# Optimization experiments

Measured on AMD Instinct MI355X. Metric: run time of the kernel, lower is better.

## Reference

```python
import jax, jax.numpy as jnp
import numpy as np

NUM_CLASSES = 21
IGNORE_INDEX = 30
ALPHA = 0.25
GAMMA = 2.0
EPS = 1e-8        # numerical-stability eps added to softmax in lasd_f
ONEHOT_EPS = 1e-6  # eps added inside label_to_one_hot_label (its default)


def _lasd(logits, target):
    # logits: (N, C, H, W), target: (N, H, W) int in [0, C-1]
    p = jax.nn.softmax(logits, axis=1) + EPS                # (N,C,H,W)
    # torch.std(dim=1) uses the unbiased estimator (ddof=1)
    sigma = jnp.std(p, axis=1, ddof=1)                       # (N,H,W)
    # min_max_scale_f: global MinMaxScaler over all elements (detached in torch)
    smin = jnp.min(sigma)
    smax = jnp.max(sigma)
    sigma = (sigma - smin) / (smax - smin)
    sigma = jax.lax.stop_gradient(sigma)  # torch path goes through .detach().numpy()
    beta = 1.0 / jnp.exp(sigma) + 1.0                        # (N,H,W)
    # one-hot with ignore_index+1 channels (+eps), then keep first NUM_CLASSES
    one_hot = jax.nn.one_hot(target, IGNORE_INDEX + 1, axis=1,
                             dtype=logits.dtype) + ONEHOT_EPS  # (N,31,H,W)
    one_hot = one_hot[:, :NUM_CLASSES]                        # (N,C,H,W)
    focal = -ALPHA * (1.0 - p) ** GAMMA * jnp.log(p)          # (N,C,H,W)
    focal = focal * beta[:, None, :, :]
    loss_tmp = one_hot * focal
    # reduction='mean': mean over batch then mean over rest == overall mean
    loss = jnp.mean(loss_tmp)
    return loss, sigma


def setup_inputs() -> dict:
    key = jax.random.key(0)
    k1, k2 = jax.random.split(key)
    inp = jax.random.normal(k1, (8, NUM_CLASSES, 512, 512), dtype=jnp.float32)
    tgt = jax.random.randint(k2, (8, 512, 512), 0, NUM_CLASSES, dtype=jnp.int32)
    return {"input": inp, "target": tgt}


def reference(input, target):
    return _lasd(input, target)
```

## Files before the change

### kernel.cpp

```cpp
#include <hip/hip_runtime.h>

#define NCLS 21
#define HW (512 * 512)
#define HW2 (HW / 2)
#define NB 8
#define NPIX (NB * HW)
#define NPIX2 (NPIX / 2)
#define NPIX4 (NPIX / 4)
#define NBLK1 (NPIX2 / 256)
#define NBLK2 (NPIX4 / 256)
#define TOTAL_ELEMS ((long long)NPIX * NCLS)


__global__ __launch_bounds__(256) void lasd_pass1(const float2* __restrict__ in2,
                                                  const int2* __restrict__ tgt2,
                                                  float2* __restrict__ sigraw2,
                                                  float2* __restrict__ S2,
                                                  float* __restrict__ bmin,
                                                  float* __restrict__ bmax) {
    int j = blockIdx.x * 256 + threadIdx.x;
    int b = j >> 17;
    int p2 = j & (HW2 - 1);
    const float2* base = in2 + ((size_t)(b * NCLS) << 17) + p2;

    float2 x[NCLS];
#pragma unroll
    for (int c = 0; c < NCLS; ++c) x[c] = base[(size_t)c << 17];

    float s0 = 0.f, s1 = 0.f;
#pragma unroll
    for (int c = 0; c < NCLS; ++c) { s0 += __expf(x[c].x); s1 += __expf(x[c].y); }
    float inv0 = 1.0f / s0, inv1 = 1.0f / s1;
    float ls0 = __logf(s0), ls1 = __logf(s1);

    int2 tt = tgt2[j];

    float sp0 = 0, sp1 = 0, q0 = 0, q1 = 0, F0 = 0, F1 = 0, ft0 = 0, ft1 = 0;
#pragma unroll
    for (int c = 0; c < NCLS; ++c) {
        float p0 = __expf(x[c].x) * inv0 + 1e-8f;
        float p1 = __expf(x[c].y) * inv1 + 1e-8f;
        float om0 = 1.0f - p0, om1 = 1.0f - p1;
        float f0 = -0.25f * om0 * om0 * (x[c].x - ls0);
        float f1 = -0.25f * om1 * om1 * (x[c].y - ls1);
        sp0 += p0; sp1 += p1;
        q0 = fmaf(p0, p0, q0); q1 = fmaf(p1, p1, q1);
        F0 += f0; F1 += f1;
        if (c == tt.x) ft0 = f0;
        if (c == tt.y) ft1 = f1;
    }

    float var0 = fmaxf(q0 - sp0 * sp0 * (1.0f / 21.0f), 0.0f);
    float var1 = fmaxf(q1 - sp1 * sp1 * (1.0f / 21.0f), 0.0f);
    float sig0 = sqrtf(var0 * (1.0f / 20.0f));
    float sig1 = sqrtf(var1 * (1.0f / 20.0f));

    float2 sg; sg.x = sig0; sg.y = sig1;
    sigraw2[j] = sg;
    float2 Sv; Sv.x = ft0 + 1e-6f * F0; Sv.y = ft1 + 1e-6f * F1;
    S2[j] = Sv;

    float lmin = fminf(sig0, sig1), lmax = fmaxf(sig0, sig1);
#pragma unroll
    for (int off = 32; off > 0; off >>= 1) {
        lmin = fminf(lmin, __shfl_down(lmin, off));
        lmax = fmaxf(lmax, __shfl_down(lmax, off));
    }
    __shared__ float smn[4], smx[4];
    int wid = threadIdx.x >> 6, lane = threadIdx.x & 63;
    if (lane == 0) { smn[wid] = lmin; smx[wid] = lmax; }
    __syncthreads();
    if (threadIdx.x == 0) {
        bmin[blockIdx.x] = fminf(fminf(smn[0], smn[1]), fminf(smn[2], smn[3]));
        bmax[blockIdx.x] = fmaxf(fmaxf(smx[0], smx[1]), fmaxf(smx[2], smx[3]));
    }
}

__global__ __launch_bounds__(256) void lasd_reduce_mm(const float* __restrict__ bmin,
                                                      const float* __restrict__ bmax,
                                                      float2* __restrict__ mm) {
    float a = 1e30f, z = -1e30f;
#pragma unroll
    for (int k = 0; k < NBLK1 / 256; ++k) {
        a = fminf(a, bmin[threadIdx.x + k * 256]);
        z = fmaxf(z, bmax[threadIdx.x + k * 256]);
    }
#pragma unroll
    for (int off = 32; off > 0; off >>= 1) {
        a = fminf(a, __shfl_down(a, off));
        z = fmaxf(z, __shfl_down(z, off));
    }
    __shared__ float smn[4], smx[4];
    int wid = threadIdx.x >> 6, lane = threadIdx.x & 63;
    if (lane == 0) { smn[wid] = a; smx[wid] = z; }
    __syncthreads();
    if (threadIdx.x == 0) {
        float2 r;
        r.x = fminf(fminf(smn[0], smn[1]), fminf(smn[2], smn[3]));
        r.y = fmaxf(fmaxf(smx[0], smx[1]), fmaxf(smx[2], smx[3]));
        *mm = r;
    }
}

__global__ __launch_bounds__(256) void lasd_pass2(const float4* __restrict__ sigraw4,
                                                  const float4* __restrict__ S4,
                                                  float* __restrict__ sig_out,
                                                  const float2* __restrict__ mm,
                                                  double* __restrict__ partial) {
    int j = blockIdx.x * 256 + threadIdx.x;
    float2 m = *mm;
    float rinv = 1.0f / (m.y - m.x);

    float4 sg = sigraw4[j];
    float4 Sv = S4[j];
    float sraw[4] = {sg.x, sg.y, sg.z, sg.w};
    float S[4] = {Sv.x, Sv.y, Sv.z, Sv.w};
    float sum = 0.0f;
#pragma unroll
    for (int k = 0; k < 4; ++k) {
        float t = (sraw[k] - m.x) * rinv;
        sig_out[4 * j + k] = t;
        sum += (__expf(-t) + 1.0f) * S[k];
    }

#pragma unroll
    for (int off = 32; off > 0; off >>= 1) sum += __shfl_down(sum, off);
    __shared__ float sh[4];
    int wid = threadIdx.x >> 6, lane = threadIdx.x & 63;
    if (lane == 0) sh[wid] = sum;
    __syncthreads();
    if (threadIdx.x == 0)
        partial[blockIdx.x] = (double)(sh[0] + sh[1] + sh[2] + sh[3]);
}

__global__ __launch_bounds__(256) void lasd_finish(const double* __restrict__ partial,
                                                   float* __restrict__ loss_out) {
    double acc = 0.0;
#pragma unroll
    for (int k = 0; k < NBLK2 / 256; ++k)
        acc += partial[threadIdx.x + k * 256];
#pragma unroll
    for (int off = 32; off > 0; off >>= 1) acc += __shfl_down(acc, off);
    __shared__ double sh[4];
    int wid = threadIdx.x >> 6, lane = threadIdx.x & 63;
    if (lane == 0) sh[wid] = acc;
    __syncthreads();
    if (threadIdx.x == 0)
        loss_out[0] = (float)((sh[0] + sh[1] + sh[2] + sh[3]) / (double)TOTAL_ELEMS);
}

extern "C" void kernel_launch(void* const* d_in, const int* in_sizes, int n_in,
                              void* d_out, int out_size, void* d_ws, size_t ws_size,
                              hipStream_t stream) {
    const float2* logits2 = (const float2*)d_in[0];
    const int2* target2 = (const int2*)d_in[1];
    float* out = (float*)d_out;
    char* ws = (char*)d_ws;

    float* bmin = (float*)(ws);
    float* bmax = (float*)(ws + 16384);
    float2* mm = (float2*)(ws + 32768);
    double* partial = (double*)(ws + 49152);
    float* sigraw = (float*)(ws + 65536);
    float* S = (float*)(ws + 65536 + (size_t)NPIX * 4);

    lasd_pass1<<<NBLK1, 256, 0, stream>>>(logits2, target2,
                                          (float2*)sigraw, (float2*)S, bmin, bmax);
    lasd_reduce_mm<<<1, 256, 0, stream>>>(bmin, bmax, mm);
    lasd_pass2<<<NBLK2, 256, 0, stream>>>((const float4*)sigraw, (const float4*)S,
                                          out + 1, mm, partial);
    lasd_finish<<<1, 256, 0, stream>>>(partial, out);
}
```

Before: 44.03 us.

## Collapse four launches into two with grid-stride pass1 and last-block reduction

Pass1 now runs a fixed grid of 2048 blocks, each looping over two pixel pairs, so there are fewer block-level min/max partials. The separate min/max reduce kernel is removed: every pass2 block redundantly reduces the 2048 partials itself. The final-sum kernel is also removed and replaced by a threadfence and atomic-counter last-block reduction. The aim is to cut kernel launch gaps and tiny single-block kernels. The cost is redundant min/max reads in every pass2 block and reliance on atomic ordering, with the counter reset done inside pass1.

```diff
diff --git a/kernel.cpp b/kernel.cpp
--- a/kernel.cpp
+++ b/kernel.cpp
@@ -7,8 +7,10 @@
 #define NPIX (NB * HW)
 #define NPIX2 (NPIX / 2)
 #define NPIX4 (NPIX / 4)
-#define NBLK1 (NPIX2 / 256)
-#define NBLK2 (NPIX4 / 256)
+#define NBLK 2048
+#define THREADS 256
+#define GSIZE1 (NBLK * THREADS)
+#define IT1 (NPIX2 / GSIZE1)
 #define TOTAL_ELEMS ((long long)NPIX * NCLS)
 
 
@@ -17,50 +19,60 @@
                                                   float2* __restrict__ sigraw2,
                                                   float2* __restrict__ S2,
                                                   float* __restrict__ bmin,
-                                                  float* __restrict__ bmax) {
-    int j = blockIdx.x * 256 + threadIdx.x;
-    int b = j >> 17;
-    int p2 = j & (HW2 - 1);
-    const float2* base = in2 + ((size_t)(b * NCLS) << 17) + p2;
+                                                  float* __restrict__ bmax,
+                                                  int* __restrict__ counter) {
+    const int tid = blockIdx.x * THREADS + threadIdx.x;
+    if (tid == 0) *counter = 0;
 
-    float2 x[NCLS];
+    float lmin = 1e30f, lmax = -1e30f;
+
 #pragma unroll
-    for (int c = 0; c < NCLS; ++c) x[c] = base[(size_t)c << 17];
+    for (int it = 0; it < IT1; ++it) {
+        int j = tid + it * GSIZE1;
+        int b = j >> 17;
+        int p2 = j & (HW2 - 1);
+        const float2* base = in2 + ((size_t)(b * NCLS) << 17) + p2;
 
-    float s0 = 0.f, s1 = 0.f;
+        float2 x[NCLS];
 #pragma unroll
-    for (int c = 0; c < NCLS; ++c) { s0 += __expf(x[c].x); s1 += __expf(x[c].y); }
-    float inv0 = 1.0f / s0, inv1 = 1.0f / s1;
-    float ls0 = __logf(s0), ls1 = __logf(s1);
+        for (int c = 0; c < NCLS; ++c) x[c] = base[(size_t)c << 17];
 
-    int2 tt = tgt2[j];
+        float s0 = 0.f, s1 = 0.f;
+#pragma unroll
+        for (int c = 0; c < NCLS; ++c) { s0 += __expf(x[c].x); s1 += __expf(x[c].y); }
+        float inv0 = 1.0f / s0, inv1 = 1.0f / s1;
+        float ls0 = __logf(s0), ls1 = __logf(s1);
 
-    float sp0 = 0, sp1 = 0, q0 = 0, q1 = 0, F0 = 0, F1 = 0, ft0 = 0, ft1 = 0;
+        int2 tt = tgt2[j];
+
+        float sp0 = 0, sp1 = 0, q0 = 0, q1 = 0, F0 = 0, F1 = 0, ft0 = 0, ft1 = 0;
 #pragma unroll
-    for (int c = 0; c < NCLS; ++c) {
-        float p0 = __expf(x[c].x) * inv0 + 1e-8f;
-        float p1 = __expf(x[c].y) * inv1 + 1e-8f;
-        float om0 = 1.0f - p0, om1 = 1.0f - p1;
-        float f0 = -0.25f * om0 * om0 * (x[c].x - ls0);
-        float f1 = -0.25f * om1 * om1 * (x[c].y - ls1);
-        sp0 += p0; sp1 += p1;
-        q0 = fmaf(p0, p0, q0); q1 = fmaf(p1, p1, q1);
-        F0 += f0; F1 += f1;
-        if (c == tt.x) ft0 = f0;
-        if (c == tt.y) ft1 = f1;
+        for (int c = 0; c < NCLS; ++c) {
+            float p0 = __expf(x[c].x) * inv0 + 1e-8f;
+            float p1 = __expf(x[c].y) * inv1 + 1e-8f;
+            float om0 = 1.0f - p0, om1 = 1.0f - p1;
+            float f0 = -0.25f * om0 * om0 * (x[c].x - ls0);
+            float f1 = -0.25f * om1 * om1 * (x[c].y - ls1);
+            sp0 += p0; sp1 += p1;
+            q0 = fmaf(p0, p0, q0); q1 = fmaf(p1, p1, q1);
+            F0 += f0; F1 += f1;
+            if (c == tt.x) ft0 = f0;
+            if (c == tt.y) ft1 = f1;
+        }
+
+        float var0 = fmaxf(q0 - sp0 * sp0 * (1.0f / 21.0f), 0.0f);
+        float var1 = fmaxf(q1 - sp1 * sp1 * (1.0f / 21.0f), 0.0f);
+        float sg0 = sqrtf(var0 * (1.0f / 20.0f));
+        float sg1 = sqrtf(var1 * (1.0f / 20.0f));
+
+        float2 sg; sg.x = sg0; sg.y = sg1;
+        sigraw2[j] = sg;
+        float2 Sv; Sv.x = ft0 + 1e-6f * F0; Sv.y = ft1 + 1e-6f * F1;
+        S2[j] = Sv;
+        lmin = fminf(lmin, fminf(sg0, sg1));
+        lmax = fmaxf(lmax, fmaxf(sg0, sg1));
     }
 
-    float var0 = fmaxf(q0 - sp0 * sp0 * (1.0f / 21.0f), 0.0f);
-    float var1 = fmaxf(q1 - sp1 * sp1 * (1.0f / 21.0f), 0.0f);
-    float sig0 = sqrtf(var0 * (1.0f / 20.0f));
-    float sig1 = sqrtf(var1 * (1.0f / 20.0f));
-
-    float2 sg; sg.x = sig0; sg.y = sig1;
-    sigraw2[j] = sg;
-    float2 Sv; Sv.x = ft0 + 1e-6f * F0; Sv.y = ft1 + 1e-6f * F1;
-    S2[j] = Sv;
-
-    float lmin = fminf(sig0, sig1), lmax = fmaxf(sig0, sig1);
 #pragma unroll
     for (int off = 32; off > 0; off >>= 1) {
         lmin = fminf(lmin, __shfl_down(lmin, off));
@@ -76,14 +88,20 @@
     }
 }
 
-__global__ __launch_bounds__(256) void lasd_reduce_mm(const float* __restrict__ bmin,
-                                                      const float* __restrict__ bmax,
-                                                      float2* __restrict__ mm) {
+__global__ __launch_bounds__(256) void lasd_pass2(const float4* __restrict__ sigraw4,
+                                                  const float4* __restrict__ S4,
+                                                  float* __restrict__ out,
+                                                  const float* __restrict__ bmin,
+                                                  const float* __restrict__ bmax,
+                                                  double* __restrict__ partial,
+                                                  int* __restrict__ counter) {
+    const int wid = threadIdx.x >> 6, lane = threadIdx.x & 63;
+
     float a = 1e30f, z = -1e30f;
 #pragma unroll
-    for (int k = 0; k < NBLK1 / 256; ++k) {
-        a = fminf(a, bmin[threadIdx.x + k * 256]);
-        z = fmaxf(z, bmax[threadIdx.x + k * 256]);
+    for (int k = 0; k < NBLK / THREADS; ++k) {
+        a = fminf(a, bmin[threadIdx.x + k * THREADS]);
+        z = fmaxf(z, bmax[threadIdx.x + k * THREADS]);
     }
 #pragma unroll
     for (int off = 32; off > 0; off >>= 1) {
@@ -91,62 +109,56 @@
         z = fmaxf(z, __shfl_down(z, off));
     }
     __shared__ float smn[4], smx[4];
-    int wid = threadIdx.x >> 6, lane = threadIdx.x & 63;
+    __shared__ float s_min, s_max;
     if (lane == 0) { smn[wid] = a; smx[wid] = z; }
     __syncthreads();
     if (threadIdx.x == 0) {
-        float2 r;
-        r.x = fminf(fminf(smn[0], smn[1]), fminf(smn[2], smn[3]));
-        r.y = fmaxf(fmaxf(smx[0], smx[1]), fmaxf(smx[2], smx[3]));
-        *mm = r;
+        s_min = fminf(fminf(smn[0], smn[1]), fminf(smn[2], smn[3]));
+        s_max = fmaxf(fmaxf(smx[0], smx[1]), fmaxf(smx[2], smx[3]));
     }
-}
+    __syncthreads();
+    float smin = s_min;
+    float rinv = 1.0f / (s_max - smin);
 
-__global__ __launch_bounds__(256) void lasd_pass2(const float4* __restrict__ sigraw4,
-                                                  const float4* __restrict__ S4,
-                                                  float* __restrict__ sig_out,
-                                                  const float2* __restrict__ mm,
-                                                  double* __restrict__ partial) {
-    int j = blockIdx.x * 256 + threadIdx.x;
-    float2 m = *mm;
-    float rinv = 1.0f / (m.y - m.x);
-
+    int j = blockIdx.x * THREADS + threadIdx.x;
     float4 sg = sigraw4[j];
     float4 Sv = S4[j];
     float sraw[4] = {sg.x, sg.y, sg.z, sg.w};
     float S[4] = {Sv.x, Sv.y, Sv.z, Sv.w};
-    float sum = 0.0f;
+    float lsum = 0.0f;
 #pragma unroll
     for (int k = 0; k < 4; ++k) {
-        float t = (sraw[k] - m.x) * rinv;
-        sig_out[4 * j + k] = t;
-        sum += (__expf(-t) + 1.0f) * S[k];
+        float t = (sraw[k] - smin) * rinv;
+        out[1 + 4 * j + k] = t;
+        lsum += (__expf(-t) + 1.0f) * S[k];
     }
+#pragma unroll
+    for (int off = 32; off > 0; off >>= 1) lsum += __shfl_down(lsum, off);
+    __shared__ float shs[4];
+    if (lane == 0) shs[wid] = lsum;
+    __syncthreads();
+    __shared__ bool s_last;
+    if (threadIdx.x == 0) {
+        partial[blockIdx.x] = (double)(shs[0] + shs[1] + shs[2] + shs[3]);
+        __threadfence();
+        int old = atomicAdd(counter, 1);
+        s_last = (old == NBLK - 1);
+    }
+    __syncthreads();
 
+    if (s_last) {
+        double acc = 0.0;
 #pragma unroll
-    for (int off = 32; off > 0; off >>= 1) sum += __shfl_down(sum, off);
-    __shared__ float sh[4];
-    int wid = threadIdx.x >> 6, lane = threadIdx.x & 63;
-    if (lane == 0) sh[wid] = sum;
-    __syncthreads();
-    if (threadIdx.x == 0)
-        partial[blockIdx.x] = (double)(sh[0] + sh[1] + sh[2] + sh[3]);
-}
-
-__global__ __launch_bounds__(256) void lasd_finish(const double* __restrict__ partial,
-                                                   float* __restrict__ loss_out) {
-    double acc = 0.0;
+        for (int k = 0; k < NBLK / THREADS; ++k)
+            acc += ((volatile const double*)partial)[threadIdx.x + k * THREADS];
 #pragma unroll
-    for (int k = 0; k < NBLK2 / 256; ++k)
-        acc += partial[threadIdx.x + k * 256];
-#pragma unroll
-    for (int off = 32; off > 0; off >>= 1) acc += __shfl_down(acc, off);
-    __shared__ double sh[4];
-    int wid = threadIdx.x >> 6, lane = threadIdx.x & 63;
-    if (lane == 0) sh[wid] = acc;
-    __syncthreads();
-    if (threadIdx.x == 0)
-        loss_out[0] = (float)((sh[0] + sh[1] + sh[2] + sh[3]) / (double)TOTAL_ELEMS);
+        for (int off = 32; off > 0; off >>= 1) acc += __shfl_down(acc, off);
+        __shared__ double shd[4];
+        if (lane == 0) shd[wid] = acc;
+        __syncthreads();
+        if (threadIdx.x == 0)
+            out[0] = (float)((shd[0] + shd[1] + shd[2] + shd[3]) / (double)TOTAL_ELEMS);
+    }
 }
 
 extern "C" void kernel_launch(void* const* d_in, const int* in_sizes, int n_in,
@@ -157,17 +169,16 @@
     float* out = (float*)d_out;
     char* ws = (char*)d_ws;
 
-    float* bmin = (float*)(ws);
-    float* bmax = (float*)(ws + 16384);
-    float2* mm = (float2*)(ws + 32768);
-    double* partial = (double*)(ws + 49152);
+    float* bmin = (float*)ws;
+    float* bmax = (float*)(ws + 8192);
+    int* counter = (int*)(ws + 16384);
+    double* partial = (double*)(ws + 16448);
     float* sigraw = (float*)(ws + 65536);
     float* S = (float*)(ws + 65536 + (size_t)NPIX * 4);
 
-    lasd_pass1<<<NBLK1, 256, 0, stream>>>(logits2, target2,
-                                          (float2*)sigraw, (float2*)S, bmin, bmax);
-    lasd_reduce_mm<<<1, 256, 0, stream>>>(bmin, bmax, mm);
-    lasd_pass2<<<NBLK2, 256, 0, stream>>>((const float4*)sigraw, (const float4*)S,
-                                          out + 1, mm, partial);
-    lasd_finish<<<1, 256, 0, stream>>>(partial, out);
+    lasd_pass1<<<NBLK, THREADS, 0, stream>>>(logits2, target2,
+                                             (float2*)sigraw, (float2*)S,
+                                             bmin, bmax, counter);
+    lasd_pass2<<<NBLK, THREADS, 0, stream>>>((const float4*)sigraw, (const float4*)S,
+                                             out, bmin, bmax, partial, counter);
 }
```

After: 104.1 us. +136.5%, slower.

## Store sigma and focal terms as packed fp16 and fold min-max reduce into pass2

Applied to the files above, without the earlier changes.

Pass1 now writes the per-pixel sigma and target focal term as one packed half2 word instead of two float arrays, halving the intermediate write and read traffic. The single-block min/max reduction kernel is removed. Every pass2 block now re-reduces all pass1 block minima and maxima itself through float4 loads, which saves one launch at the cost of redundant work per block. The half-precision intermediates lose accuracy in the sigma output and in the loss.

```diff
diff --git a/kernel.cpp b/kernel.cpp
--- a/kernel.cpp
+++ b/kernel.cpp
@@ -1,4 +1,5 @@
 #include <hip/hip_runtime.h>
+#include <hip/hip_fp16.h>
 
 #define NCLS 21
 #define HW (512 * 512)
@@ -12,10 +13,11 @@
 #define TOTAL_ELEMS ((long long)NPIX * NCLS)
 
 
+union HU { __half2 h; unsigned int u; };
+
 __global__ __launch_bounds__(256) void lasd_pass1(const float2* __restrict__ in2,
                                                   const int2* __restrict__ tgt2,
-                                                  float2* __restrict__ sigraw2,
-                                                  float2* __restrict__ S2,
+                                                  uint2* __restrict__ sigS2,
                                                   float* __restrict__ bmin,
                                                   float* __restrict__ bmax) {
     int j = blockIdx.x * 256 + threadIdx.x;
@@ -52,15 +54,19 @@
 
     float var0 = fmaxf(q0 - sp0 * sp0 * (1.0f / 21.0f), 0.0f);
     float var1 = fmaxf(q1 - sp1 * sp1 * (1.0f / 21.0f), 0.0f);
-    float sig0 = sqrtf(var0 * (1.0f / 20.0f));
-    float sig1 = sqrtf(var1 * (1.0f / 20.0f));
+    float sg0 = sqrtf(var0 * (1.0f / 20.0f));
+    float sg1 = sqrtf(var1 * (1.0f / 20.0f));
+    float S0 = ft0 + 1e-6f * F0;
+    float S1 = ft1 + 1e-6f * F1;
 
-    float2 sg; sg.x = sig0; sg.y = sig1;
-    sigraw2[j] = sg;
-    float2 Sv; Sv.x = ft0 + 1e-6f * F0; Sv.y = ft1 + 1e-6f * F1;
-    S2[j] = Sv;
+    HU h0, h1;
+    h0.h.x = __float2half_rn(sg0); h0.h.y = __float2half_rn(S0);
+    h1.h.x = __float2half_rn(sg1); h1.h.y = __float2half_rn(S1);
+    uint2 pk; pk.x = h0.u; pk.y = h1.u;
+    sigS2[j] = pk;
 
-    float lmin = fminf(sig0, sig1), lmax = fmaxf(sig0, sig1);
+    float r0 = __half2float(h0.h.x), r1 = __half2float(h1.h.x);
+    float lmin = fminf(r0, r1), lmax = fmaxf(r0, r1);
 #pragma unroll
     for (int off = 32; off > 0; off >>= 1) {
         lmin = fminf(lmin, __shfl_down(lmin, off));
@@ -76,14 +82,20 @@
     }
 }
 
-__global__ __launch_bounds__(256) void lasd_reduce_mm(const float* __restrict__ bmin,
-                                                      const float* __restrict__ bmax,
-                                                      float2* __restrict__ mm) {
+__global__ __launch_bounds__(256) void lasd_pass2(const uint4* __restrict__ sigS4,
+                                                  float* __restrict__ out,
+                                                  const float4* __restrict__ bmin4,
+                                                  const float4* __restrict__ bmax4,
+                                                  double* __restrict__ partial) {
+    const int wid = threadIdx.x >> 6, lane = threadIdx.x & 63;
+
     float a = 1e30f, z = -1e30f;
 #pragma unroll
-    for (int k = 0; k < NBLK1 / 256; ++k) {
-        a = fminf(a, bmin[threadIdx.x + k * 256]);
-        z = fmaxf(z, bmax[threadIdx.x + k * 256]);
+    for (int k = 0; k < NBLK1 / 4 / 256; ++k) {
+        float4 v = bmin4[threadIdx.x + k * 256];
+        float4 w = bmax4[threadIdx.x + k * 256];
+        a = fminf(a, fminf(fminf(v.x, v.y), fminf(v.z, v.w)));
+        z = fmaxf(z, fmaxf(fmaxf(w.x, w.y), fmaxf(w.z, w.w)));
     }
 #pragma unroll
     for (int off = 32; off > 0; off >>= 1) {
@@ -91,46 +103,38 @@
         z = fmaxf(z, __shfl_down(z, off));
     }
     __shared__ float smn[4], smx[4];
-    int wid = threadIdx.x >> 6, lane = threadIdx.x & 63;
+    __shared__ float s_min, s_rinv;
     if (lane == 0) { smn[wid] = a; smx[wid] = z; }
     __syncthreads();
     if (threadIdx.x == 0) {
-        float2 r;
-        r.x = fminf(fminf(smn[0], smn[1]), fminf(smn[2], smn[3]));
-        r.y = fmaxf(fmaxf(smx[0], smx[1]), fmaxf(smx[2], smx[3]));
-        *mm = r;
+        float mn = fminf(fminf(smn[0], smn[1]), fminf(smn[2], smn[3]));
+        float mx = fmaxf(fmaxf(smx[0], smx[1]), fmaxf(smx[2], smx[3]));
+        s_min = mn;
+        s_rinv = 1.0f / (mx - mn);
     }
-}
+    __syncthreads();
+    float smin = s_min, rinv = s_rinv;
 
-__global__ __launch_bounds__(256) void lasd_pass2(const float4* __restrict__ sigraw4,
-                                                  const float4* __restrict__ S4,
-                                                  float* __restrict__ sig_out,
-                                                  const float2* __restrict__ mm,
-                                                  double* __restrict__ partial) {
     int j = blockIdx.x * 256 + threadIdx.x;
-    float2 m = *mm;
-    float rinv = 1.0f / (m.y - m.x);
-
-    float4 sg = sigraw4[j];
-    float4 Sv = S4[j];
-    float sraw[4] = {sg.x, sg.y, sg.z, sg.w};
-    float S[4] = {Sv.x, Sv.y, Sv.z, Sv.w};
-    float sum = 0.0f;
+    uint4 pk = sigS4[j];
+    unsigned int w[4] = {pk.x, pk.y, pk.z, pk.w};
+    float lsum = 0.0f;
 #pragma unroll
     for (int k = 0; k < 4; ++k) {
-        float t = (sraw[k] - m.x) * rinv;
-        sig_out[4 * j + k] = t;
-        sum += (__expf(-t) + 1.0f) * S[k];
+        HU cv; cv.u = w[k];
+        float sg = __half2float(cv.h.x);
+        float S = __half2float(cv.h.y);
+        float t = (sg - smin) * rinv;
+        out[1 + 4 * j + k] = t;
+        lsum += (__expf(-t) + 1.0f) * S;
     }
-
 #pragma unroll
-    for (int off = 32; off > 0; off >>= 1) sum += __shfl_down(sum, off);
-    __shared__ float sh[4];
-    int wid = threadIdx.x >> 6, lane = threadIdx.x & 63;
-    if (lane == 0) sh[wid] = sum;
+    for (int off = 32; off > 0; off >>= 1) lsum += __shfl_down(lsum, off);
+    __shared__ float shs[4];
+    if (lane == 0) shs[wid] = lsum;
     __syncthreads();
     if (threadIdx.x == 0)
-        partial[blockIdx.x] = (double)(sh[0] + sh[1] + sh[2] + sh[3]);
+        partial[blockIdx.x] = (double)(shs[0] + shs[1] + shs[2] + shs[3]);
 }
 
 __global__ __launch_bounds__(256) void lasd_finish(const double* __restrict__ partial,
@@ -157,17 +161,14 @@
     float* out = (float*)d_out;
     char* ws = (char*)d_ws;
 
-    float* bmin = (float*)(ws);
+    float* bmin = (float*)ws;
     float* bmax = (float*)(ws + 16384);
-    float2* mm = (float2*)(ws + 32768);
-    double* partial = (double*)(ws + 49152);
-    float* sigraw = (float*)(ws + 65536);
-    float* S = (float*)(ws + 65536 + (size_t)NPIX * 4);
+    double* partial = (double*)(ws + 32768);
+    uint2* sigS = (uint2*)(ws + 65536);
 
-    lasd_pass1<<<NBLK1, 256, 0, stream>>>(logits2, target2,
-                                          (float2*)sigraw, (float2*)S, bmin, bmax);
-    lasd_reduce_mm<<<1, 256, 0, stream>>>(bmin, bmax, mm);
-    lasd_pass2<<<NBLK2, 256, 0, stream>>>((const float4*)sigraw, (const float4*)S,
-                                          out + 1, mm, partial);
+    lasd_pass1<<<NBLK1, 256, 0, stream>>>(logits2, target2, sigS, bmin, bmax);
+    lasd_pass2<<<NBLK2, 256, 0, stream>>>((const uint4*)sigS, out,
+                                          (const float4*)bmin, (const float4*)bmax,
+                                          partial);
     lasd_finish<<<1, 256, 0, stream>>>(partial, out);
 }
```

New measurement: 41.85 us. 1.05x faster.
